# Kernel optimization log

Hardware: AMD Instinct MI355X
Metric: run time of the kernel (lower is better)

## Reference

```python
import jax, jax.numpy as jnp
import numpy as np

B, N, H = 32, 1024, 512
DT = 0.1  # euler step size = t[1]-t[0] for torchdiffeq euler on t=[0.0,0.1]

def setup_inputs() -> dict:
    key = jax.random.key(0)
    ks = jax.random.split(key, 8)
    s = 1.0 / np.sqrt(2 * H)
    return {
        "inp": jax.random.normal(ks[0], (B, N, H), jnp.float32),
        "hz": jax.random.normal(ks[1], (B, N, H), jnp.float32),
        # func1: tanh(Linear(2H -> 2H)) ODE dynamics
        "Wf": jax.random.uniform(ks[2], (2 * H, 2 * H), jnp.float32, -s, s),
        "bf": jnp.zeros((2 * H,), jnp.float32),
        # mlp head: Linear(2H,2H) -> ReLU -> Linear(2H,H) -> Tanh
        "W1": jax.random.uniform(ks[3], (2 * H, 2 * H), jnp.float32, -s, s),
        "b1": jnp.zeros((2 * H,), jnp.float32),
        "W2": jax.random.uniform(ks[4], (2 * H, H), jnp.float32, -s, s),
        "b2": jnp.zeros((H,), jnp.float32),
    }

def reference(inp, hz, Wf, bf, W1, b1, W2, b2):
    # h0 = cat([input, hz], -1)  -> [B, N, 2H]
    h = jnp.concatenate([inp, hz], axis=-1)
    def func1(h):  # dh/dt (time-independent dynamics)
        return jnp.tanh(h @ Wf + bf)
    # two odeint calls, each a single fixed euler step over t=[0.0, 0.1]
    for _ in range(2):
        h = h + DT * func1(h)
    # MLP head
    h = jax.nn.relu(h @ W1 + b1)
    h = jnp.tanh(h @ W2 + b2)
    return h  # [B, N, H]
```

## Files before the change

### kernel.cpp

```cpp
#include <hip/hip_runtime.h>
#include <hip/hip_bf16.h>

typedef __attribute__((ext_vector_type(8))) short short8;
typedef __attribute__((ext_vector_type(4))) float floatx4;

__device__ __forceinline__ ushort f2bf(float x) {
    __hip_bfloat16 h = __float2bfloat16(x);
    return __builtin_bit_cast(ushort, h);
}
__device__ __forceinline__ float bf2f(ushort u) {
    __hip_bfloat16 h = __builtin_bit_cast(__hip_bfloat16, u);
    return __bfloat162float(h);
}

__device__ __forceinline__ float fast_tanh(float z) {
    float e = __expf(2.0f * z);
    return 1.0f - 2.0f * __builtin_amdgcn_rcpf(e + 1.0f);
}

__device__ __forceinline__ void gload_lds16(const ushort* g, ushort* l) {
    __builtin_amdgcn_global_load_lds(
        (const __attribute__((address_space(1))) unsigned int*)(const void*)g,
        (__attribute__((address_space(3))) unsigned int*)(void*)l,
        16, 0, 0);
}

__global__ void prep(const float* __restrict__ inp, const float* __restrict__ hz,
                     const float* __restrict__ Wf, const float* __restrict__ W1,
                     const float* __restrict__ W2,
                     ushort* __restrict__ h0, ushort* __restrict__ WfT,
                     ushort* __restrict__ W1T, ushort* __restrict__ W2T) {
    int bid = blockIdx.x;
    int tid = threadIdx.x;
    __shared__ float tile[32][33];
    if (bid < 32768) {
        const float* src = (bid < 16384) ? inp : hz;
        int half = (bid < 16384) ? 0 : 1;
        int b = bid - half * 16384;
        size_t i = ((size_t)b * 256 + tid) * 4;
        size_t row = i >> 9;
        int col = (int)(i & 511);
        float4 v = *(const float4*)(src + i);
        ushort4 o = make_ushort4(f2bf(v.x), f2bf(v.y), f2bf(v.z), f2bf(v.w));
        *(ushort4*)(h0 + row * 1024 + half * 512 + col) = o;
    } else {
        int t = bid - 32768;
        const float* W;
        ushort* WT;
        int K = 1024, N = 1024;
        if (t < 1024)      { W = Wf; WT = WfT; }
        else if (t < 2048) { W = W1; WT = W1T; t -= 1024; }
        else               { W = W2; WT = W2T; t -= 2048; N = 512; }
        int tx = tid & 31, ty = tid >> 5;
        int nb = (t % (N / 32)) * 32, kb = (t / (N / 32)) * 32;
        #pragma unroll
        for (int j = ty; j < 32; j += 8)
            tile[j][tx] = W[(size_t)(kb + j) * N + nb + tx];
        __syncthreads();
        #pragma unroll
        for (int j = ty; j < 32; j += 8)
            WT[(size_t)(nb + j) * K + kb + tx] = f2bf(tile[tx][j]);
    }
}

template <int MODE, int NOUT, int NX>
__global__ __launch_bounds__(512, 2) void gemm_ep(
    const ushort* __restrict__ A, const ushort* __restrict__ BT,
    const float* __restrict__ bias,
    ushort* __restrict__ outB, float* __restrict__ outF) {
    constexpr int K = 1024;
    __shared__ ushort As[4][8192];
    __shared__ ushort Bs[4][8192];

    const int tid = threadIdx.x;
    const int wave = tid >> 6, lane = tid & 63;

    const int id = blockIdx.x;
    const int inner = id >> 3;
    const int nTile = inner % NX;
    const int mTile = (id & 7) * 16 + inner / NX;
    const int mBase = mTile * 256;
    const int nBase = nTile * 256;
    const int waveM = wave >> 2;
    const int waveN = wave & 3;

    const int c = wave * 64 + lane;
    const int ra = c >> 2;
    const int qa = (c & 3) ^ ((ra >> 1) & 3);
    const ushort* agA0 = A  + (size_t)(mBase + ra) * K + qa * 8;
    const ushort* agA1 = A  + (size_t)(mBase + 128 + ra) * K + qa * 8;
    const ushort* bgB0 = BT + (size_t)(nBase + ra) * K + qa * 8;
    const ushort* bgB1 = BT + (size_t)(nBase + 128 + ra) * K + qa * 8;
    ushort* asD = &As[0][0] + wave * 512;
    ushort* bsD = &Bs[0][0] + wave * 512;

    floatx4 acc[8][4];
    #pragma unroll
    for (int i = 0; i < 8; i++)
        #pragma unroll
        for (int j = 0; j < 4; j++) acc[i][j] = (floatx4)(0.f);

    const int mrow = lane & 15;
    const int g = lane >> 4;
    const int pq = g ^ ((mrow >> 1) & 3);
    const ushort* aB = &As[0][0] + (waveM * 128 + mrow) * 32 + pq * 8;
    const ushort* bB = &Bs[0][0] + (waveN * 64 + mrow) * 32 + pq * 8;

#define MFMA_ROW(MT, AF)                                                            \
    acc[MT][0] = __builtin_amdgcn_mfma_f32_16x16x32_bf16(AF, bf0, acc[MT][0], 0,0,0); \
    acc[MT][1] = __builtin_amdgcn_mfma_f32_16x16x32_bf16(AF, bf1, acc[MT][1], 0,0,0); \
    acc[MT][2] = __builtin_amdgcn_mfma_f32_16x16x32_bf16(AF, bf2, acc[MT][2], 0,0,0); \
    acc[MT][3] = __builtin_amdgcn_mfma_f32_16x16x32_bf16(AF, bf3, acc[MT][3], 0,0,0);

#define PANEL(T, STG, VMASM)                                                   \
  {                                                                            \
    const int s  = (T) & 3;                                                    \
    const int s3 = ((T) + 3) & 3;                                              \
           \
    short8 af0 = *(const short8*)(aB + s * 8192 + 0 * 512);                    \
    short8 af1 = *(const short8*)(aB + s * 8192 + 1 * 512);                    \
    short8 af2 = *(const short8*)(aB + s * 8192 + 2 * 512);                    \
    short8 af3 = *(const short8*)(aB + s * 8192 + 3 * 512);                    \
    short8 bf0 = *(const short8*)(bB + s * 8192 + 0 * 512);                    \
    short8 bf1 = *(const short8*)(bB + s * 8192 + 1 * 512);                    \
    short8 bf2 = *(const short8*)(bB + s * 8192 + 2 * 512);                    \
    short8 bf3 = *(const short8*)(bB + s * 8192 + 3 * 512);                    \
    if (STG) {                                                                 \
      gload_lds16(agA0 + ((T) + 3) * 32, asD + s3 * 8192);                     \
      gload_lds16(agA1 + ((T) + 3) * 32, asD + s3 * 8192 + 4096);              \
    }                                                                          \
    asm volatile("s_waitcnt lgkmcnt(0)" ::: "memory");                         \
    __builtin_amdgcn_sched_barrier(0);                                         \
    __builtin_amdgcn_s_setprio(1);                                             \
    MFMA_ROW(0, af0) MFMA_ROW(1, af1) MFMA_ROW(2, af2) MFMA_ROW(3, af3)        \
    __builtin_amdgcn_s_setprio(0);                                             \
           \
    af0 = *(const short8*)(aB + s * 8192 + 2048 + 0 * 512);                    \
    af1 = *(const short8*)(aB + s * 8192 + 2048 + 1 * 512);                    \
    af2 = *(const short8*)(aB + s * 8192 + 2048 + 2 * 512);                    \
    af3 = *(const short8*)(aB + s * 8192 + 2048 + 3 * 512);                    \
    if (STG) {                                                                 \
      gload_lds16(bgB0 + ((T) + 3) * 32, bsD + s3 * 8192);                     \
      gload_lds16(bgB1 + ((T) + 3) * 32, bsD + s3 * 8192 + 4096);              \
    }                                                                          \
    asm volatile(VMASM ::: "memory");                                          \
    __builtin_amdgcn_s_barrier();            \
    asm volatile("s_waitcnt lgkmcnt(0)" ::: "memory");                         \
    __builtin_amdgcn_sched_barrier(0);                                         \
    __builtin_amdgcn_s_setprio(1);                                             \
    MFMA_ROW(4, af0) MFMA_ROW(5, af1) MFMA_ROW(6, af2) MFMA_ROW(7, af3)        \
    __builtin_amdgcn_s_setprio(0);                                             \
    __builtin_amdgcn_sched_barrier(0);                                         \
    __builtin_amdgcn_s_barrier();            \
  }

    #pragma unroll
    for (int p = 0; p < 3; ++p) {
        gload_lds16(agA0 + p * 32, asD + p * 8192);
        gload_lds16(agA1 + p * 32, asD + p * 8192 + 4096);
        gload_lds16(bgB0 + p * 32, bsD + p * 8192);
        gload_lds16(bgB1 + p * 32, bsD + p * 8192 + 4096);
    }
    asm volatile("s_waitcnt vmcnt(8)" ::: "memory");
    __builtin_amdgcn_s_barrier();

    for (int tt = 0; tt < 7; ++tt) {
        const int t4 = tt * 4;
        PANEL(t4 + 0, true, "s_waitcnt vmcnt(8)")
        PANEL(t4 + 1, true, "s_waitcnt vmcnt(8)")
        PANEL(t4 + 2, true, "s_waitcnt vmcnt(8)")
        PANEL(t4 + 3, true, "s_waitcnt vmcnt(8)")
    }
    PANEL(28, true,  "s_waitcnt vmcnt(8)")
    PANEL(29, false, "s_waitcnt vmcnt(4)")
    PANEL(30, false, "s_waitcnt vmcnt(0)")
    PANEL(31, false, "s_waitcnt vmcnt(0)")

#undef PANEL
#undef MFMA_ROW

    const int col0 = nBase + waveN * 64 + (lane & 15);
    const int row0 = mBase + waveM * 128 + (lane >> 4) * 4;
    #pragma unroll
    for (int mt = 0; mt < 8; mt++) {
        #pragma unroll
        for (int nt = 0; nt < 4; nt++) {
            const int col = col0 + nt * 16;
            const float bv = bias[col];
            #pragma unroll
            for (int r = 0; r < 4; r++) {
                const int row = row0 + mt * 16 + r;
                const float z = acc[mt][nt][r] + bv;
                if (MODE == 1) {
                    float carry = bf2f(A[(size_t)row * K + col]);
                    outB[(size_t)row * NOUT + col] = f2bf(carry + 0.1f * fast_tanh(z));
                } else if (MODE == 2) {
                    outB[(size_t)row * NOUT + col] = f2bf(fmaxf(z, 0.f));
                } else {
                    outF[(size_t)row * NOUT + col] = fast_tanh(z);
                }
            }
        }
    }
}

extern "C" void kernel_launch(void* const* d_in, const int* in_sizes, int n_in,
                              void* d_out, int out_size, void* d_ws, size_t ws_size,
                              hipStream_t stream) {
    const float* inp = (const float*)d_in[0];
    const float* hz  = (const float*)d_in[1];
    const float* Wf  = (const float*)d_in[2];
    const float* bf_ = (const float*)d_in[3];
    const float* W1  = (const float*)d_in[4];
    const float* b1  = (const float*)d_in[5];
    const float* W2  = (const float*)d_in[6];
    const float* b2  = (const float*)d_in[7];
    float* out = (float*)d_out;

    char* ws = (char*)d_ws;
    ushort* WfT  = (ushort*)(ws);
    ushort* W1T  = (ushort*)(ws + (size_t)(2 << 20));
    ushort* W2T  = (ushort*)(ws + (size_t)(4 << 20));
    ushort* bufA = (ushort*)(ws + (size_t)(8 << 20));
    ushort* bufB = (ushort*)(ws + (size_t)(8 << 20) + ((size_t)64 << 20));

    prep<<<35328, 256, 0, stream>>>(inp, hz, Wf, W1, W2, bufA, WfT, W1T, W2T);

    gemm_ep<1, 1024, 4><<<512, 512, 0, stream>>>(bufA, WfT, bf_, bufB, nullptr);
    gemm_ep<1, 1024, 4><<<512, 512, 0, stream>>>(bufB, WfT, bf_, bufA, nullptr);
    gemm_ep<2, 1024, 4><<<512, 512, 0, stream>>>(bufA, W1T, b1, bufB, nullptr);
    gemm_ep<3, 512, 2><<<256, 512, 0, stream>>>(bufB, W2T, b2, nullptr, out);
}
```

Measured before the change: 425.7 us.

## Double-buffer LDS fragment registers to prefetch next panel during MFMAs

Adds register double-buffering of the A/B LDS fragments: the next panel's first-half A and B fragments are read right after the barrier of the current panel and overlap with the second-half MFMAs. The lgkmcnt waits are relaxed to partial counts so LDS reads overlap compute. The aim is to hide LDS read latency before each MFMA block. In exchange it needs roughly 16 more VGPRs for the extra fragment buffers, which may reduce occupancy or cause spills, and the partial wait counts must exactly match the order in which reads are issued.

```diff
diff --git a/kernel.cpp b/kernel.cpp
--- a/kernel.cpp
+++ b/kernel.cpp
@@ -106,49 +106,56 @@
     const ushort* aB = &As[0][0] + (waveM * 128 + mrow) * 32 + pq * 8;
     const ushort* bB = &Bs[0][0] + (waveN * 64 + mrow) * 32 + pq * 8;
 
-#define MFMA_ROW(MT, AF)                                                            \
-    acc[MT][0] = __builtin_amdgcn_mfma_f32_16x16x32_bf16(AF, bf0, acc[MT][0], 0,0,0); \
-    acc[MT][1] = __builtin_amdgcn_mfma_f32_16x16x32_bf16(AF, bf1, acc[MT][1], 0,0,0); \
-    acc[MT][2] = __builtin_amdgcn_mfma_f32_16x16x32_bf16(AF, bf2, acc[MT][2], 0,0,0); \
-    acc[MT][3] = __builtin_amdgcn_mfma_f32_16x16x32_bf16(AF, bf3, acc[MT][3], 0,0,0);
-
-#define PANEL(T, STG, VMASM)                                                   \
+    short8 ca0[4], cb0[4], ca1[4], cb1[4], cz[4];
+
+#define MFMA4(MT, AF, CBARR)                                                          \
+    acc[MT][0] = __builtin_amdgcn_mfma_f32_16x16x32_bf16(AF, CBARR[0], acc[MT][0],0,0,0); \
+    acc[MT][1] = __builtin_amdgcn_mfma_f32_16x16x32_bf16(AF, CBARR[1], acc[MT][1],0,0,0); \
+    acc[MT][2] = __builtin_amdgcn_mfma_f32_16x16x32_bf16(AF, CBARR[2], acc[MT][2],0,0,0); \
+    acc[MT][3] = __builtin_amdgcn_mfma_f32_16x16x32_bf16(AF, CBARR[3], acc[MT][3],0,0,0);
+
+#define PANEL(T, CA, CB, NA, NB, STG, NXT, VMASM, LGASM)                       \
   {                                                                            \
     const int s  = (T) & 3;                                                    \
+    const int s1 = ((T) + 1) & 3;                                              \
     const int s3 = ((T) + 3) & 3;                                              \
-           \
-    short8 af0 = *(const short8*)(aB + s * 8192 + 0 * 512);                    \
-    short8 af1 = *(const short8*)(aB + s * 8192 + 1 * 512);                    \
-    short8 af2 = *(const short8*)(aB + s * 8192 + 2 * 512);                    \
-    short8 af3 = *(const short8*)(aB + s * 8192 + 3 * 512);                    \
-    short8 bf0 = *(const short8*)(bB + s * 8192 + 0 * 512);                    \
-    short8 bf1 = *(const short8*)(bB + s * 8192 + 1 * 512);                    \
-    short8 bf2 = *(const short8*)(bB + s * 8192 + 2 * 512);                    \
-    short8 bf3 = *(const short8*)(bB + s * 8192 + 3 * 512);                    \
+         \
+    cz[0] = *(const short8*)(aB + s * 8192 + 2048 + 0 * 512);                  \
+    cz[1] = *(const short8*)(aB + s * 8192 + 2048 + 1 * 512);                  \
+    cz[2] = *(const short8*)(aB + s * 8192 + 2048 + 2 * 512);                  \
+    cz[3] = *(const short8*)(aB + s * 8192 + 2048 + 3 * 512);                  \
     if (STG) {                                                                 \
       gload_lds16(agA0 + ((T) + 3) * 32, asD + s3 * 8192);                     \
       gload_lds16(agA1 + ((T) + 3) * 32, asD + s3 * 8192 + 4096);              \
     }                                                                          \
-    asm volatile("s_waitcnt lgkmcnt(0)" ::: "memory");                         \
+    asm volatile("s_waitcnt lgkmcnt(4)" ::: "memory");                         \
     __builtin_amdgcn_sched_barrier(0);                                         \
     __builtin_amdgcn_s_setprio(1);                                             \
-    MFMA_ROW(0, af0) MFMA_ROW(1, af1) MFMA_ROW(2, af2) MFMA_ROW(3, af3)        \
+    MFMA4(0, CA[0], CB) MFMA4(1, CA[1], CB)                                    \
+    MFMA4(2, CA[2], CB) MFMA4(3, CA[3], CB)                                    \
     __builtin_amdgcn_s_setprio(0);                                             \
-           \
-    af0 = *(const short8*)(aB + s * 8192 + 2048 + 0 * 512);                    \
-    af1 = *(const short8*)(aB + s * 8192 + 2048 + 1 * 512);                    \
-    af2 = *(const short8*)(aB + s * 8192 + 2048 + 2 * 512);                    \
-    af3 = *(const short8*)(aB + s * 8192 + 2048 + 3 * 512);                    \
+          \
     if (STG) {                                                                 \
       gload_lds16(bgB0 + ((T) + 3) * 32, bsD + s3 * 8192);                     \
       gload_lds16(bgB1 + ((T) + 3) * 32, bsD + s3 * 8192 + 4096);              \
     }                                                                          \
     asm volatile(VMASM ::: "memory");                                          \
-    __builtin_amdgcn_s_barrier();            \
-    asm volatile("s_waitcnt lgkmcnt(0)" ::: "memory");                         \
+    __builtin_amdgcn_s_barrier();         \
+    if (NXT) {                                                                 \
+      NA[0] = *(const short8*)(aB + s1 * 8192 + 0 * 512);                      \
+      NA[1] = *(const short8*)(aB + s1 * 8192 + 1 * 512);                      \
+      NA[2] = *(const short8*)(aB + s1 * 8192 + 2 * 512);                      \
+      NA[3] = *(const short8*)(aB + s1 * 8192 + 3 * 512);                      \
+      NB[0] = *(const short8*)(bB + s1 * 8192 + 0 * 512);                      \
+      NB[1] = *(const short8*)(bB + s1 * 8192 + 1 * 512);                      \
+      NB[2] = *(const short8*)(bB + s1 * 8192 + 2 * 512);                      \
+      NB[3] = *(const short8*)(bB + s1 * 8192 + 3 * 512);                      \
+    }                                                                          \
+    asm volatile(LGASM ::: "memory");                                          \
     __builtin_amdgcn_sched_barrier(0);                                         \
     __builtin_amdgcn_s_setprio(1);                                             \
-    MFMA_ROW(4, af0) MFMA_ROW(5, af1) MFMA_ROW(6, af2) MFMA_ROW(7, af3)        \
+    MFMA4(4, cz[0], CB) MFMA4(5, cz[1], CB)                                    \
+    MFMA4(6, cz[2], CB) MFMA4(7, cz[3], CB)                                    \
     __builtin_amdgcn_s_setprio(0);                                             \
     __builtin_amdgcn_sched_barrier(0);                                         \
     __builtin_amdgcn_s_barrier();            \
@@ -163,21 +170,29 @@
     }
     asm volatile("s_waitcnt vmcnt(8)" ::: "memory");
     __builtin_amdgcn_s_barrier();
+    ca0[0] = *(const short8*)(aB + 0 * 512);
+    ca0[1] = *(const short8*)(aB + 1 * 512);
+    ca0[2] = *(const short8*)(aB + 2 * 512);
+    ca0[3] = *(const short8*)(aB + 3 * 512);
+    cb0[0] = *(const short8*)(bB + 0 * 512);
+    cb0[1] = *(const short8*)(bB + 1 * 512);
+    cb0[2] = *(const short8*)(bB + 2 * 512);
+    cb0[3] = *(const short8*)(bB + 3 * 512);
 
     for (int tt = 0; tt < 7; ++tt) {
         const int t4 = tt * 4;
-        PANEL(t4 + 0, true, "s_waitcnt vmcnt(8)")
-        PANEL(t4 + 1, true, "s_waitcnt vmcnt(8)")
-        PANEL(t4 + 2, true, "s_waitcnt vmcnt(8)")
-        PANEL(t4 + 3, true, "s_waitcnt vmcnt(8)")
-    }
-    PANEL(28, true,  "s_waitcnt vmcnt(8)")
-    PANEL(29, false, "s_waitcnt vmcnt(4)")
-    PANEL(30, false, "s_waitcnt vmcnt(0)")
-    PANEL(31, false, "s_waitcnt vmcnt(0)")
+        PANEL(t4 + 0, ca0, cb0, ca1, cb1, true, true, "s_waitcnt vmcnt(8)", "s_waitcnt lgkmcnt(8)")
+        PANEL(t4 + 1, ca1, cb1, ca0, cb0, true, true, "s_waitcnt vmcnt(8)", "s_waitcnt lgkmcnt(8)")
+        PANEL(t4 + 2, ca0, cb0, ca1, cb1, true, true, "s_waitcnt vmcnt(8)", "s_waitcnt lgkmcnt(8)")
+        PANEL(t4 + 3, ca1, cb1, ca0, cb0, true, true, "s_waitcnt vmcnt(8)", "s_waitcnt lgkmcnt(8)")
+    }
+    PANEL(28, ca0, cb0, ca1, cb1, true,  true,  "s_waitcnt vmcnt(8)", "s_waitcnt lgkmcnt(8)")
+    PANEL(29, ca1, cb1, ca0, cb0, false, true,  "s_waitcnt vmcnt(4)", "s_waitcnt lgkmcnt(8)")
+    PANEL(30, ca0, cb0, ca1, cb1, false, true,  "s_waitcnt vmcnt(0)", "s_waitcnt lgkmcnt(8)")
+    PANEL(31, ca1, cb1, ca0, cb0, false, false, "s_waitcnt vmcnt(0)", "s_waitcnt lgkmcnt(0)")
 
 #undef PANEL
-#undef MFMA_ROW
+#undef MFMA4
 
     const int col0 = nBase + waveN * 64 + (lane & 15);
     const int row0 = mBase + waveM * 128 + (lane >> 4) * 4;
```

After: 436.4 us. 2.5% more time.

## Fuse prep and four GEMM phases into one cooperative persistent kernel

Applied to the files above, without the earlier changes.

Replaces five separate launches (input and weight prep plus four GEMMs) with a single cooperative kernel of 256 blocks. Phases are separated by grid.sync, and each block loops over GEMM tile jobs. This removes per-launch overhead and inter-kernel gaps. In exchange it adds grid-wide barriers, runs the prep work with fewer threads, and leaves phase 3 with only one job per block, so its parallelism is unchanged but the kernel may lose per-kernel tuning and occupancy.

```diff
diff --git a/kernel.cpp b/kernel.cpp
--- a/kernel.cpp
+++ b/kernel.cpp
@@ -1,5 +1,8 @@
 #include <hip/hip_runtime.h>
 #include <hip/hip_bf16.h>
+#include <hip/hip_cooperative_groups.h>
+
+namespace cg = cooperative_groups;
 
 typedef __attribute__((ext_vector_type(8))) short short8;
 typedef __attribute__((ext_vector_type(4))) float floatx4;
@@ -25,84 +28,67 @@
         16, 0, 0);
 }
 
-__global__ void prep(const float* __restrict__ inp, const float* __restrict__ hz,
-                     const float* __restrict__ Wf, const float* __restrict__ W1,
-                     const float* __restrict__ W2,
-                     ushort* __restrict__ h0, ushort* __restrict__ WfT,
-                     ushort* __restrict__ W1T, ushort* __restrict__ W2T) {
-    int bid = blockIdx.x;
-    int tid = threadIdx.x;
-    __shared__ float tile[32][33];
-    if (bid < 32768) {
-        const float* src = (bid < 16384) ? inp : hz;
-        int half = (bid < 16384) ? 0 : 1;
-        int b = bid - half * 16384;
-        size_t i = ((size_t)b * 256 + tid) * 4;
-        size_t row = i >> 9;
-        int col = (int)(i & 511);
-        float4 v = *(const float4*)(src + i);
-        ushort4 o = make_ushort4(f2bf(v.x), f2bf(v.y), f2bf(v.z), f2bf(v.w));
-        *(ushort4*)(h0 + row * 1024 + half * 512 + col) = o;
-    } else {
-        int t = bid - 32768;
-        const float* W;
-        ushort* WT;
-        int K = 1024, N = 1024;
-        if (t < 1024)      { W = Wf; WT = WfT; }
-        else if (t < 2048) { W = W1; WT = W1T; t -= 1024; }
-        else               { W = W2; WT = W2T; t -= 2048; N = 512; }
-        int tx = tid & 31, ty = tid >> 5;
-        int nb = (t % (N / 32)) * 32, kb = (t / (N / 32)) * 32;
-        #pragma unroll
-        for (int j = ty; j < 32; j += 8)
-            tile[j][tx] = W[(size_t)(kb + j) * N + nb + tx];
-        __syncthreads();
-        #pragma unroll
-        for (int j = ty; j < 32; j += 8)
-            WT[(size_t)(nb + j) * K + kb + tx] = f2bf(tile[tx][j]);
-    }
-}
-
-template <int MODE, int NOUT, int NX>
-__global__ __launch_bounds__(512, 2) void gemm_ep(
-    const ushort* __restrict__ A, const ushort* __restrict__ BT,
-    const float* __restrict__ bias,
-    ushort* __restrict__ outB, float* __restrict__ outF) {
-    constexpr int K = 1024;
+__global__ __launch_bounds__(512, 2) void fused(
+    const float* __restrict__ inp, const float* __restrict__ hz,
+    const float* __restrict__ Wf,  const float* __restrict__ W1,
+    const float* __restrict__ W2,  const float* __restrict__ bfb,
+    const float* __restrict__ b1,  const float* __restrict__ b2,
+    ushort* __restrict__ WfT, ushort* __restrict__ W1T, ushort* __restrict__ W2T,
+    ushort* __restrict__ bufA, ushort* __restrict__ bufB, float* __restrict__ out)
+{
     __shared__ ushort As[4][8192];
     __shared__ ushort Bs[4][8192];
 
+    cg::grid_group grid = cg::this_grid();
     const int tid = threadIdx.x;
+    const int bid = blockIdx.x;
     const int wave = tid >> 6, lane = tid & 63;
 
-    const int id = blockIdx.x;
-    const int inner = id >> 3;
-    const int nTile = inner % NX;
-    const int mTile = (id & 7) * 16 + inner / NX;
-    const int mBase = mTile * 256;
-    const int nBase = nTile * 256;
+    {
+        int u = bid * 512 + tid;
+        #pragma unroll 2
+        for (int it = 0; it < 64; ++it, u += 131072) {
+            const int isHz = (u >= 4194304) ? 1 : 0;
+            const float* src = isHz ? hz : inp;
+            const int v = isHz ? (u - 4194304) : u;
+            const size_t i = (size_t)v * 4;
+            const size_t row = i >> 9;
+            const int col = (int)(i & 511);
+            float4 x = *(const float4*)(src + i);
+            ushort4 o = make_ushort4(f2bf(x.x), f2bf(x.y), f2bf(x.z), f2bf(x.w));
+            *(ushort4*)(bufA + row * 1024 + isHz * 512 + col) = o;
+        }
+        float* tl = (float*)&As[0][0];
+        const int tx = tid & 31, ty = tid >> 5;
+        for (int t = bid; t < 2560; t += 256) {
+            int t2 = t; const float* W; ushort* WT; int N = 1024;
+            if (t2 < 1024)      { W = Wf; WT = WfT; }
+            else if (t2 < 2048) { W = W1; WT = W1T; t2 -= 1024; }
+            else                { W = W2; WT = W2T; t2 -= 2048; N = 512; }
+            const int nb = (t2 % (N / 32)) * 32, kb = (t2 / (N / 32)) * 32;
+            __syncthreads();
+            #pragma unroll
+            for (int j = ty; j < 32; j += 16)
+                tl[j * 33 + tx] = W[(size_t)(kb + j) * N + nb + tx];
+            __syncthreads();
+            #pragma unroll
+            for (int j = ty; j < 32; j += 16)
+                WT[(size_t)(nb + j) * 1024 + kb + tx] = f2bf(tl[tx * 33 + j]);
+        }
+    }
+    __threadfence();
+    grid.sync();
+
     const int waveM = wave >> 2;
     const int waveN = wave & 3;
-
     const int c = wave * 64 + lane;
     const int ra = c >> 2;
     const int qa = (c & 3) ^ ((ra >> 1) & 3);
-    const ushort* agA0 = A  + (size_t)(mBase + ra) * K + qa * 8;
-    const ushort* agA1 = A  + (size_t)(mBase + 128 + ra) * K + qa * 8;
-    const ushort* bgB0 = BT + (size_t)(nBase + ra) * K + qa * 8;
-    const ushort* bgB1 = BT + (size_t)(nBase + 128 + ra) * K + qa * 8;
-    ushort* asD = &As[0][0] + wave * 512;
-    ushort* bsD = &Bs[0][0] + wave * 512;
-
-    floatx4 acc[8][4];
-    #pragma unroll
-    for (int i = 0; i < 8; i++)
-        #pragma unroll
-        for (int j = 0; j < 4; j++) acc[i][j] = (floatx4)(0.f);
-
     const int mrow = lane & 15;
     const int g = lane >> 4;
     const int pq = g ^ ((mrow >> 1) & 3);
+    ushort* asD = &As[0][0] + wave * 512;
+    ushort* bsD = &Bs[0][0] + wave * 512;
     const ushort* aB = &As[0][0] + (waveM * 128 + mrow) * 32 + pq * 8;
     const ushort* bB = &Bs[0][0] + (waveN * 64 + mrow) * 32 + pq * 8;
 
@@ -116,7 +102,7 @@
   {                                                                            \
     const int s  = (T) & 3;                                                    \
     const int s3 = ((T) + 3) & 3;                                              \
-           \
+                     \
     short8 af0 = *(const short8*)(aB + s * 8192 + 0 * 512);                    \
     short8 af1 = *(const short8*)(aB + s * 8192 + 1 * 512);                    \
     short8 af2 = *(const short8*)(aB + s * 8192 + 2 * 512);                    \
@@ -134,7 +120,7 @@
     __builtin_amdgcn_s_setprio(1);                                             \
     MFMA_ROW(0, af0) MFMA_ROW(1, af1) MFMA_ROW(2, af2) MFMA_ROW(3, af3)        \
     __builtin_amdgcn_s_setprio(0);                                             \
-           \
+                     \
     af0 = *(const short8*)(aB + s * 8192 + 2048 + 0 * 512);                    \
     af1 = *(const short8*)(aB + s * 8192 + 2048 + 1 * 512);                    \
     af2 = *(const short8*)(aB + s * 8192 + 2048 + 2 * 512);                    \
@@ -154,54 +140,83 @@
     __builtin_amdgcn_s_barrier();            \
   }
 
-    #pragma unroll
-    for (int p = 0; p < 3; ++p) {
-        gload_lds16(agA0 + p * 32, asD + p * 8192);
-        gload_lds16(agA1 + p * 32, asD + p * 8192 + 4096);
-        gload_lds16(bgB0 + p * 32, bsD + p * 8192);
-        gload_lds16(bgB1 + p * 32, bsD + p * 8192 + 4096);
-    }
-    asm volatile("s_waitcnt vmcnt(8)" ::: "memory");
-    __builtin_amdgcn_s_barrier();
-
-    for (int tt = 0; tt < 7; ++tt) {
-        const int t4 = tt * 4;
-        PANEL(t4 + 0, true, "s_waitcnt vmcnt(8)")
-        PANEL(t4 + 1, true, "s_waitcnt vmcnt(8)")
-        PANEL(t4 + 2, true, "s_waitcnt vmcnt(8)")
-        PANEL(t4 + 3, true, "s_waitcnt vmcnt(8)")
-    }
-    PANEL(28, true,  "s_waitcnt vmcnt(8)")
-    PANEL(29, false, "s_waitcnt vmcnt(4)")
-    PANEL(30, false, "s_waitcnt vmcnt(0)")
-    PANEL(31, false, "s_waitcnt vmcnt(0)")
-
-#undef PANEL
-#undef MFMA_ROW
-
-    const int col0 = nBase + waveN * 64 + (lane & 15);
-    const int row0 = mBase + waveM * 128 + (lane >> 4) * 4;
-    #pragma unroll
-    for (int mt = 0; mt < 8; mt++) {
-        #pragma unroll
-        for (int nt = 0; nt < 4; nt++) {
-            const int col = col0 + nt * 16;
-            const float bv = bias[col];
-            #pragma unroll
-            for (int r = 0; r < 4; r++) {
-                const int row = row0 + mt * 16 + r;
-                const float z = acc[mt][nt][r] + bv;
-                if (MODE == 1) {
-                    float carry = bf2f(A[(size_t)row * K + col]);
-                    outB[(size_t)row * NOUT + col] = f2bf(carry + 0.1f * fast_tanh(z));
-                } else if (MODE == 2) {
-                    outB[(size_t)row * NOUT + col] = f2bf(fmaxf(z, 0.f));
-                } else {
-                    outF[(size_t)row * NOUT + col] = fast_tanh(z);
+    for (int ph = 0; ph < 4; ++ph) {
+        const ushort* Ap; const ushort* BTp; const float* biasp;
+        ushort* oB; float* oF; int mode, NOUT, nxlog, nJobs;
+        if (ph == 0)      { Ap = bufA; BTp = WfT; biasp = bfb; oB = bufB; oF = nullptr; mode = 1; NOUT = 1024; nxlog = 2; nJobs = 512; }
+        else if (ph == 1) { Ap = bufB; BTp = WfT; biasp = bfb; oB = bufA; oF = nullptr; mode = 1; NOUT = 1024; nxlog = 2; nJobs = 512; }
+        else if (ph == 2) { Ap = bufA; BTp = W1T; biasp = b1;  oB = bufB; oF = nullptr; mode = 2; NOUT = 1024; nxlog = 2; nJobs = 512; }
+        else              { Ap = bufB; BTp = W2T; biasp = b2;  oB = nullptr; oF = out;  mode = 3; NOUT = 512;  nxlog = 1; nJobs = 256; }
+
+        for (int job = bid; job < nJobs; job += 256) {
+            const int inner = job >> 3;
+            const int nTile = inner & ((1 << nxlog) - 1);
+            const int mTile = (job & 7) * 16 + (inner >> nxlog);
+            const int mBase = mTile * 256;
+            const int nBase = nTile * 256;
+
+            const ushort* agA0 = Ap  + (size_t)(mBase + ra) * 1024 + qa * 8;
+            const ushort* agA1 = Ap  + (size_t)(mBase + 128 + ra) * 1024 + qa * 8;
+            const ushort* bgB0 = BTp + (size_t)(nBase + ra) * 1024 + qa * 8;
+            const ushort* bgB1 = BTp + (size_t)(nBase + 128 + ra) * 1024 + qa * 8;
+
+            floatx4 acc[8][4];
+            #pragma unroll
+            for (int i = 0; i < 8; i++)
+                #pragma unroll
+                for (int j = 0; j < 4; j++) acc[i][j] = (floatx4)(0.f);
+
+            #pragma unroll
+            for (int p = 0; p < 3; ++p) {
+                gload_lds16(agA0 + p * 32, asD + p * 8192);
+                gload_lds16(agA1 + p * 32, asD + p * 8192 + 4096);
+                gload_lds16(bgB0 + p * 32, bsD + p * 8192);
+                gload_lds16(bgB1 + p * 32, bsD + p * 8192 + 4096);
+            }
+            asm volatile("s_waitcnt vmcnt(8)" ::: "memory");
+            __builtin_amdgcn_s_barrier();
+
+            for (int tt = 0; tt < 7; ++tt) {
+                const int t4 = tt * 4;
+                PANEL(t4 + 0, true, "s_waitcnt vmcnt(8)")
+                PANEL(t4 + 1, true, "s_waitcnt vmcnt(8)")
+                PANEL(t4 + 2, true, "s_waitcnt vmcnt(8)")
+                PANEL(t4 + 3, true, "s_waitcnt vmcnt(8)")
+            }
+            PANEL(28, true,  "s_waitcnt vmcnt(8)")
+            PANEL(29, false, "s_waitcnt vmcnt(4)")
+            PANEL(30, false, "s_waitcnt vmcnt(0)")
+            PANEL(31, false, "s_waitcnt vmcnt(0)")
+
+            const int col0 = nBase + waveN * 64 + (lane & 15);
+            const int row0 = mBase + waveM * 128 + (lane >> 4) * 4;
+            #pragma unroll
+            for (int mt = 0; mt < 8; mt++) {
+                #pragma unroll
+                for (int nt = 0; nt < 4; nt++) {
+                    const int col = col0 + nt * 16;
+                    const float bv = biasp[col];
+                    #pragma unroll
+                    for (int r = 0; r < 4; r++) {
+                        const int row = row0 + mt * 16 + r;
+                        const float z = acc[mt][nt][r] + bv;
+                        if (mode == 1) {
+                            float carry = bf2f(Ap[(size_t)row * 1024 + col]);
+                            oB[(size_t)row * NOUT + col] = f2bf(carry + 0.1f * fast_tanh(z));
+                        } else if (mode == 2) {
+                            oB[(size_t)row * NOUT + col] = f2bf(fmaxf(z, 0.f));
+                        } else {
+                            oF[(size_t)row * NOUT + col] = fast_tanh(z);
+                        }
+                    }
                 }
             }
         }
+        __threadfence();
+        grid.sync();
     }
+#undef PANEL
+#undef MFMA_ROW
 }
 
 extern "C" void kernel_launch(void* const* d_in, const int* in_sizes, int n_in,
@@ -224,10 +239,10 @@
     ushort* bufA = (ushort*)(ws + (size_t)(8 << 20));
     ushort* bufB = (ushort*)(ws + (size_t)(8 << 20) + ((size_t)64 << 20));
 
-    prep<<<35328, 256, 0, stream>>>(inp, hz, Wf, W1, W2, bufA, WfT, W1T, W2T);
-
-    gemm_ep<1, 1024, 4><<<512, 512, 0, stream>>>(bufA, WfT, bf_, bufB, nullptr);
-    gemm_ep<1, 1024, 4><<<512, 512, 0, stream>>>(bufB, WfT, bf_, bufA, nullptr);
-    gemm_ep<2, 1024, 4><<<512, 512, 0, stream>>>(bufA, W1T, b1, bufB, nullptr);
-    gemm_ep<3, 512, 2><<<256, 512, 0, stream>>>(bufB, W2T, b2, nullptr, out);
-}
+    void* args[] = { (void*)&inp, (void*)&hz, (void*)&Wf, (void*)&W1, (void*)&W2,
+                     (void*)&bf_, (void*)&b1, (void*)&b2,
+                     (void*)&WfT, (void*)&W1T, (void*)&W2T,
+                     (void*)&bufA, (void*)&bufB, (void*)&out };
+    hipLaunchCooperativeKernel((const void*)fused, dim3(256), dim3(512),
+                               args, 0, stream);
+}
```

Result: slower. 986.8 us (+131.8%).
